# Performance work log

Hardware: AMD Instinct MI355X
Metric: run time of the kernel (lower is better)

## Reference

```python
import jax, jax.numpy as jnp
import numpy as np

NUM_HEADS = 16
EMBED_DIM = 128
SEQ_LEN = 1024
BATCH = 4


def setup_inputs() -> dict:
    key = jax.random.key(0)
    ks = jax.random.split(key, 5)
    x = jax.random.normal(ks[0], (BATCH, SEQ_LEN, EMBED_DIM), dtype=jnp.float32)
    scale = 0.02
    w_q = jax.random.normal(ks[1], (NUM_HEADS * EMBED_DIM, EMBED_DIM), dtype=jnp.float32) * scale
    w_k = jax.random.normal(ks[2], (NUM_HEADS * EMBED_DIM, EMBED_DIM), dtype=jnp.float32) * scale
    w_v = jax.random.normal(ks[3], (NUM_HEADS * EMBED_DIM, EMBED_DIM), dtype=jnp.float32) * scale
    w_o = jax.random.normal(ks[4], (EMBED_DIM, NUM_HEADS * EMBED_DIM), dtype=jnp.float32) * scale
    return {"x": x, "w_q": w_q, "w_k": w_k, "w_v": w_v, "w_o": w_o}


def _rope_tables(seq_len, embed_dim, dtype):
    half = embed_dim // 2
    # faithful to source: angles = 10000 ** (2*i / embed_dim)  (positive exponent)
    angles = jnp.power(jnp.asarray(10000.0, dtype), 2.0 * jnp.arange(half, dtype=dtype) / embed_dim)
    theta = jnp.arange(seq_len, dtype=dtype)[:, None] * angles[None, :]  # [S, half]
    return jnp.cos(theta), jnp.sin(theta)


def _apply_rope(t, cos, sin):
    # t: [B, S, H, E] viewed as complex pairs on last dim
    B, S, H, E = t.shape
    tr = t.reshape(B, S, H, E // 2, 2)
    a, b = tr[..., 0], tr[..., 1]
    c = cos[None, :, None, :]
    s = sin[None, :, None, :]
    out = jnp.stack([a * c - b * s, a * s + b * c], axis=-1)
    return out.reshape(B, S, H, E)


def reference(x, w_q, w_k, w_v, w_o):
    B, S, E = x.shape
    H = NUM_HEADS
    q = jnp.einsum('bse,fe->bsf', x, w_q).reshape(B, S, H, E)
    k = jnp.einsum('bse,fe->bsf', x, w_k).reshape(B, S, H, E)
    v = jnp.einsum('bse,fe->bsf', x, w_v).reshape(B, S, H, E)
    cos, sin = _rope_tables(S, E, x.dtype)
    q = _apply_rope(q, cos, sin)
    k = _apply_rope(k, cos, sin)
    att = jnp.einsum('bqhd,bkhd->bhqk', q, k) / jnp.sqrt(jnp.asarray(E, x.dtype))
    causal = jnp.tril(jnp.ones((S, S), dtype=bool))[None, None]
    att = jnp.where(causal, att, jnp.asarray(-jnp.inf, x.dtype))
    att = jax.nn.softmax(att, axis=-1)
    y = jnp.einsum('bhqk,bkhd->bqhd', att, v).reshape(B, S, H * E)
    return jnp.einsum('bsf,ef->bse', y, w_o)
```

## Files before the change

kernel.cpp:

```cpp
#include <hip/hip_runtime.h>

typedef unsigned short u16;
typedef unsigned int   u32;
typedef __attribute__((ext_vector_type(8))) short bf8_t;
typedef __attribute__((ext_vector_type(4))) float f4_t;

#define SEQ   1024
#define NH    16
#define DH    128
#define BATCH 4
#define MROWS 4096
#define FDIM  2048

__device__ __forceinline__ u16 f2bf(float f) {
  union { float f; u32 u; } v; v.f = f;
  u32 u = v.u;
  u += 0x7fffu + ((u >> 16) & 1u);
  return (u16)(u >> 16);
}

__global__ __launch_bounds__(256) void to_bf16(
    const float* __restrict__ x,  const float* __restrict__ wq,
    const float* __restrict__ wk, const float* __restrict__ wv,
    const float* __restrict__ wo,
    u16* __restrict__ xb, u16* __restrict__ wqb, u16* __restrict__ wkb,
    u16* __restrict__ wvb, u16* __restrict__ wob) {
  int i = blockIdx.x * 256 + threadIdx.x;
  const float* s; u16* d; int o;
  if      (i <  65536) { s = x;  d = xb;  o = i; }
  else if (i <  98304) { s = wq; d = wqb; o = i - 65536; }
  else if (i < 131072) { s = wk; d = wkb; o = i - 98304; }
  else if (i < 163840) { s = wv; d = wvb; o = i - 131072; }
  else                 { s = wo; d = wob; o = i - 163840; }
  const f4_t* sp = reinterpret_cast<const f4_t*>(s + (size_t)o * 8);
  f4_t a = sp[0], b = sp[1];
  bf8_t pk;
#pragma unroll
  for (int j = 0; j < 4; ++j) { pk[j] = (short)f2bf(a[j]); pk[4 + j] = (short)f2bf(b[j]); }
  *reinterpret_cast<bf8_t*>(d + (size_t)o * 8) = pk;
}

__global__ __launch_bounds__(256) void rope_tables(float* __restrict__ cosT,
                                                   float* __restrict__ sinT) {
  int i = blockIdx.x * 256 + threadIdx.x;
  int s = i >> 6, p = i & 63;
  float ef = (float)(2 * p) / 128.0f;
  float angf = (float)pow(10000.0, (double)ef);
  float thf  = (float)s * angf;
  cosT[i] = cosf(thf);
  sinT[i] = sinf(thf);
}

__global__ __launch_bounds__(256) void qkv_rope(
    const u16* __restrict__ xb,
    const u16* __restrict__ wqb, const u16* __restrict__ wkb,
    const u16* __restrict__ wvb,
    const float* __restrict__ cosT, const float* __restrict__ sinT,
    u16* __restrict__ qo, u16* __restrict__ ko, u16* __restrict__ vo) {
  __shared__ __align__(16) u16 a_lds[64 * 128];
  __shared__ __align__(16) u16 b_lds[64 * 128];
  const int tid = threadIdx.x;
  const int mt = blockIdx.x;
  const int by = blockIdx.y;
  const int mat = by >> 5;
  const int nt  = by & 31;
  const u16* w = (mat == 0) ? wqb : ((mat == 1) ? wkb : wvb);
  const int m0 = mt * 64, n0 = nt * 64;

#pragma unroll
  for (int i = 0; i < 4; ++i) {
    int idx = tid + i * 256;
    int row = idx >> 4, e0 = (idx & 15) * 8;
    int hw = ((row << 7) | e0) ^ ((row & 7) << 3);
    bf8_t xa = *reinterpret_cast<const bf8_t*>(xb + (size_t)(m0 + row) * 128 + e0);
    *reinterpret_cast<bf8_t*>(&a_lds[hw]) = xa;
    bf8_t wa = *reinterpret_cast<const bf8_t*>(w + (size_t)(n0 + row) * 128 + e0);
    *reinterpret_cast<bf8_t*>(&b_lds[hw]) = wa;
  }
  __syncthreads();

  const int lane = tid & 63, wid = tid >> 6;
  const int wr = wid >> 1, wc = wid & 1;
  const int g = lane >> 4, c16 = lane & 15;
  f4_t acc[2][2];
#pragma unroll
  for (int a = 0; a < 2; ++a)
#pragma unroll
    for (int b = 0; b < 2; ++b) acc[a][b] = (f4_t)0.0f;

#pragma unroll
  for (int kc = 0; kc < 4; ++kc) {
    bf8_t af[2], bf_[2];
#pragma unroll
    for (int fr = 0; fr < 2; ++fr) {
      int row = wr * 32 + fr * 16 + c16;
      int hw = ((row << 7) | (kc * 32 + g * 8)) ^ ((row & 7) << 3);
      af[fr] = *reinterpret_cast<const bf8_t*>(&a_lds[hw]);
    }
#pragma unroll
    for (int fc = 0; fc < 2; ++fc) {
      int row = wc * 32 + fc * 16 + c16;
      int hw = ((row << 7) | (kc * 32 + g * 8)) ^ ((row & 7) << 3);
      bf_[fc] = *reinterpret_cast<const bf8_t*>(&b_lds[hw]);
    }
#pragma unroll
    for (int fr = 0; fr < 2; ++fr)
#pragma unroll
      for (int fc = 0; fc < 2; ++fc)
        acc[fr][fc] = __builtin_amdgcn_mfma_f32_16x16x32_bf16(af[fr], bf_[fc], acc[fr][fc], 0, 0, 0);
  }

  if (mat == 2) {
    __syncthreads();
#pragma unroll
    for (int fr = 0; fr < 2; ++fr)
#pragma unroll
      for (int fc = 0; fc < 2; ++fc)
#pragma unroll
        for (int j = 0; j < 4; ++j) {
          int fcol = wc * 32 + fc * 16 + c16;
          int m = wr * 32 + fr * 16 + g * 4 + j;
          a_lds[fcol * 72 + m] = f2bf(acc[fr][fc][j]);
        }
    __syncthreads();
    const int b = mt >> 4, sl0 = m0 & 1023;
    const int hq = nt >> 1, dvb = (nt & 1) * 64;
#pragma unroll
    for (int i = 0; i < 2; ++i) {
      int r = tid >> 2, c0 = ((tid & 3) * 2 + i) * 8;
      bf8_t v = *reinterpret_cast<const bf8_t*>(&a_lds[r * 72 + c0]);
      size_t adr = ((size_t)((b * 16 + hq) * 128 + dvb + r)) * 1024 + sl0 + c0;
      *reinterpret_cast<bf8_t*>(vo + adr) = v;
    }
    return;
  }

  u16* outp = (mat == 0) ? qo : ko;
#pragma unroll
  for (int fr = 0; fr < 2; ++fr) {
#pragma unroll
    for (int fc = 0; fc < 2; ++fc) {
      int fcol = n0 + wc * 32 + fc * 16 + c16;
      int h = fcol >> 7, d = fcol & 127, p = d >> 1;
#pragma unroll
      for (int j = 0; j < 4; ++j) {
        int m = m0 + wr * 32 + fr * 16 + g * 4 + j;
        int b = m >> 10, sl = m & 1023;
        float v = acc[fr][fc][j];
        float vx = __shfl_xor(v, 1);
        float cv = cosT[sl * 64 + p], sv = sinT[sl * 64 + p];
        if (!(lane & 1)) {
          float e_out = v * cv - vx * sv;
          float o_out = v * sv + vx * cv;
          u32 u = (u32)f2bf(e_out) | ((u32)f2bf(o_out) << 16);
          u32 elem = ((u32)((b * 16 + h) * 1024 + sl)) * 128 + (u32)d;
          reinterpret_cast<u32*>(outp)[elem >> 1] = u;
        }
      }
    }
  }
}

__device__ __forceinline__ void stage_kv(const u16* __restrict__ Kp,
                                         const u16* __restrict__ Vt, int t,
                                         int tid, u16* k_lds, u16* vT) {
#pragma unroll
  for (int i = 0; i < 4; ++i) {
    int n = tid >> 2, c0 = ((tid & 3) * 4 + i) * 8;
    bf8_t kv = *reinterpret_cast<const bf8_t*>(Kp + (size_t)(t * 64 + n) * 128 + c0);
    *reinterpret_cast<bf8_t*>(&k_lds[n * 128 + (c0 ^ ((n & 7) << 3))]) = kv;
    int dv = tid >> 1, c1 = ((tid & 1) * 4 + i) * 8;
    bf8_t vv = *reinterpret_cast<const bf8_t*>(Vt + (size_t)dv * 1024 + t * 64 + c1);
    *reinterpret_cast<bf8_t*>(&vT[dv * 72 + c1]) = vv;
  }
}

__global__ __launch_bounds__(256, 3) void attn(
    const u16* __restrict__ qw, const u16* __restrict__ kw,
    const u16* __restrict__ vtg, u16* __restrict__ yw) {
  __shared__ __align__(16) u16 k_lds[64 * 128];
  __shared__ __align__(16) u16 vT[144 * 72];
  __shared__ __align__(16) u16 p_lds[4][16 * 64];
  const int tid = threadIdx.x, lane = tid & 63, wid = tid >> 6;
  const int g = lane >> 4, c16 = lane & 15;
  const int bid = blockIdx.x;
  const int pp = 15 - (bid >> 6);
  const int bh = bid & 63;
  const int b = bh >> 4, h = bh & 15;
  const int qt = 2 * pp + (wid >> 1);
  const int T = pp + 1;
  const u16* Qp = qw + (size_t)bh * SEQ * DH;
  const u16* Kp = kw + (size_t)bh * SEQ * DH;
  const u16* Vt = vtg + (size_t)bh * DH * SEQ;
  const float kscale = 0.08838834764831845f * 1.4426950408889634f;
  const int qrow0 = qt * 32 + (wid & 1) * 16;
  const int moff = (wid >> 1) * 32 + (wid & 1) * 16;

  {
    int r = 128 + (tid >> 4), c0 = (tid & 15) * 4;
    u16 v = (r == 128) ? (u16)0x3F80 : (u16)0;
#pragma unroll
    for (int e = 0; e < 4; ++e) vT[r * 72 + c0 + e] = v;
  }

  bf8_t qf[4];
#pragma unroll
  for (int c = 0; c < 4; ++c)
    qf[c] = *reinterpret_cast<const bf8_t*>(Qp + (size_t)(qrow0 + c16) * 128 + c * 32 + g * 8);

  f4_t yacc[9];
#pragma unroll
  for (int f = 0; f < 9; ++f) yacc[f] = (f4_t)0.0f;
  float m_run[4];
#pragma unroll
  for (int j = 0; j < 4; ++j) m_run[j] = -3e38f;

  stage_kv(Kp, Vt, 0, tid, k_lds, vT);
  __syncthreads();

  for (int t = 0; t < T; ++t) {
    f4_t sf[4];
#pragma unroll
    for (int nf = 0; nf < 4; ++nf) sf[nf] = (f4_t)0.0f;
    __builtin_amdgcn_s_setprio(1);
#pragma unroll
    for (int nf = 0; nf < 4; ++nf) {
      int row = nf * 16 + c16;
#pragma unroll
      for (int kc = 0; kc < 4; ++kc) {
        int hw = ((row << 7) | (kc * 32 + g * 8)) ^ ((row & 7) << 3);
        bf8_t kf = *reinterpret_cast<const bf8_t*>(&k_lds[hw]);
        sf[nf] = __builtin_amdgcn_mfma_f32_16x16x32_bf16(qf[kc], kf, sf[nf], 0, 0, 0);
      }
    }
    __builtin_amdgcn_s_setprio(0);

    if (t == T - 1) {
#pragma unroll
      for (int nf = 0; nf < 4; ++nf) {
        int keyc = nf * 16 + c16;
#pragma unroll
        for (int j = 0; j < 4; ++j)
          if (keyc > moff + g * 4 + j) sf[nf][j] = -3e38f;
      }
    }

    int chk = 0;
#pragma unroll
    for (int j = 0; j < 4; ++j) {
      float lmx = fmaxf(fmaxf(sf[0][j], sf[1][j]), fmaxf(sf[2][j], sf[3][j]));
      chk |= (lmx > m_run[j] + 32.0f) ? 1 : 0;
    }
    if (__any(chk)) {
      float lm[4];
#pragma unroll
      for (int j = 0; j < 4; ++j) {
        lm[j] = fmaxf(fmaxf(sf[0][j], sf[1][j]), fmaxf(sf[2][j], sf[3][j]));
        lm[j] = fmaxf(lm[j], __shfl_xor(lm[j], 1));
        lm[j] = fmaxf(lm[j], __shfl_xor(lm[j], 2));
        lm[j] = fmaxf(lm[j], __shfl_xor(lm[j], 4));
        lm[j] = fmaxf(lm[j], __shfl_xor(lm[j], 8));
      }
#pragma unroll
      for (int j = 0; j < 4; ++j) {
        float mn = fmaxf(m_run[j], lm[j]);
        float alpha = exp2f((m_run[j] - mn) * kscale);
        m_run[j] = mn;
#pragma unroll
        for (int f = 0; f < 9; ++f) yacc[f][j] *= alpha;
      }
    }

#pragma unroll
    for (int nf = 0; nf < 4; ++nf) {
#pragma unroll
      for (int j = 0; j < 4; ++j) {
        float pv = exp2f((sf[nf][j] - m_run[j]) * kscale);
        int q = g * 4 + j, n = nf * 16 + c16;
        int hw = ((q << 6) | n) ^ ((q & 7) << 3);
        p_lds[wid][hw] = f2bf(pv);
      }
    }
    bf8_t pa[2];
#pragma unroll
    for (int cc = 0; cc < 2; ++cc) {
      int hw = ((c16 << 6) | (cc * 32 + g * 8)) ^ ((c16 & 7) << 3);
      pa[cc] = *reinterpret_cast<const bf8_t*>(&p_lds[wid][hw]);
    }

    __builtin_amdgcn_s_setprio(1);
#pragma unroll
    for (int f = 0; f < 9; ++f) {
#pragma unroll
      for (int cc = 0; cc < 2; ++cc) {
        bf8_t vf = *reinterpret_cast<const bf8_t*>(&vT[(f * 16 + c16) * 72 + cc * 32 + g * 8]);
        yacc[f] = __builtin_amdgcn_mfma_f32_16x16x32_bf16(pa[cc], vf, yacc[f], 0, 0, 0);
      }
    }
    __builtin_amdgcn_s_setprio(0);

    __syncthreads();
    if (t + 1 < T) {
      stage_kv(Kp, Vt, t + 1, tid, k_lds, vT);
      __syncthreads();
    }
  }

  float rl[4];
#pragma unroll
  for (int j = 0; j < 4; ++j) {
    float lv = __shfl(yacc[8][j], lane & 48);
    rl[j] = 1.0f / lv;
  }
#pragma unroll
  for (int f = 0; f < 8; ++f) {
#pragma unroll
    for (int j = 0; j < 4; ++j) {
      float yv = yacc[f][j] * rl[j];
      float yn = __shfl_xor(yv, 1);
      if (!(lane & 1)) {
        int s_ = qrow0 + g * 4 + j;
        int dv = f * 16 + c16;
        u32 u = (u32)f2bf(yv) | ((u32)f2bf(yn) << 16);
        u32 elem = ((u32)(b * 1024 + s_)) * 2048 + (u32)(h * 128 + dv);
        reinterpret_cast<u32*>(yw)[elem >> 1] = u;
      }
    }
  }
}

__global__ __launch_bounds__(256) void oproj(
    const u16* __restrict__ yw, const u16* __restrict__ wob,
    float* __restrict__ out) {
  __shared__ __align__(16) u16 a_lds[64 * 64];
  __shared__ __align__(16) u16 b_lds[64 * 64];
  const int tid = threadIdx.x, lane = tid & 63, wid = tid >> 6;
  const int g = lane >> 4, c16 = lane & 15;
  const int wr = wid >> 1, wc = wid & 1;
  const int m0 = blockIdx.x * 64, n0 = blockIdx.y * 64;
  const int z = blockIdx.z;
  f4_t acc[2][2];
#pragma unroll
  for (int a = 0; a < 2; ++a)
#pragma unroll
    for (int b = 0; b < 2; ++b) acc[a][b] = (f4_t)0.0f;

  for (int kt = z * 16; kt < z * 16 + 16; ++kt) {
    int kb = kt * 64;
#pragma unroll
    for (int i = 0; i < 2; ++i) {
      int idx = tid + i * 256;
      int row = idx >> 3, k0 = (idx & 7) * 8;
      int hw = ((row << 6) | k0) ^ ((row & 7) << 3);
      bf8_t av = *reinterpret_cast<const bf8_t*>(yw + (size_t)(m0 + row) * 2048 + kb + k0);
      *reinterpret_cast<bf8_t*>(&a_lds[hw]) = av;
      bf8_t bv = *reinterpret_cast<const bf8_t*>(wob + (size_t)(n0 + row) * 2048 + kb + k0);
      *reinterpret_cast<bf8_t*>(&b_lds[hw]) = bv;
    }
    __syncthreads();
#pragma unroll
    for (int c = 0; c < 2; ++c) {
      bf8_t af[2], bf_[2];
#pragma unroll
      for (int fr = 0; fr < 2; ++fr) {
        int row = wr * 32 + fr * 16 + c16;
        int hw = ((row << 6) | (c * 32 + g * 8)) ^ ((row & 7) << 3);
        af[fr] = *reinterpret_cast<const bf8_t*>(&a_lds[hw]);
      }
#pragma unroll
      for (int fc = 0; fc < 2; ++fc) {
        int row = wc * 32 + fc * 16 + c16;
        int hw = ((row << 6) | (c * 32 + g * 8)) ^ ((row & 7) << 3);
        bf_[fc] = *reinterpret_cast<const bf8_t*>(&b_lds[hw]);
      }
#pragma unroll
      for (int fr = 0; fr < 2; ++fr)
#pragma unroll
        for (int fc = 0; fc < 2; ++fc)
          acc[fr][fc] = __builtin_amdgcn_mfma_f32_16x16x32_bf16(af[fr], bf_[fc], acc[fr][fc], 0, 0, 0);
    }
    __syncthreads();
  }
#pragma unroll
  for (int fr = 0; fr < 2; ++fr)
#pragma unroll
    for (int fc = 0; fc < 2; ++fc)
#pragma unroll
      for (int j = 0; j < 4; ++j) {
        int m = m0 + wr * 32 + fr * 16 + g * 4 + j;
        int e = n0 + wc * 32 + fc * 16 + c16;
        atomicAdd(&out[(size_t)m * 128 + e], acc[fr][fc][j]);
      }
}

extern "C" void kernel_launch(void* const* d_in, const int* in_sizes, int n_in,
                              void* d_out, int out_size, void* d_ws, size_t ws_size,
                              hipStream_t stream) {
  const float* x  = (const float*)d_in[0];
  const float* wq = (const float*)d_in[1];
  const float* wk = (const float*)d_in[2];
  const float* wv = (const float*)d_in[3];
  const float* wo = (const float*)d_in[4];
  float* out = (float*)d_out;

  char* ws = (char*)d_ws;
  const size_t NEED = (512ull << 10) + 4ull * (16ull << 20) + (3ull << 20);
  if (ws_size < NEED) return;
  float* cosT = (float*)ws;
  float* sinT = cosT + 64 * 1024;
  u16* qws = (u16*)(ws + (512 << 10));
  u16* kws = qws + (8u << 20);
  u16* vws = kws + (8u << 20);
  u16* yws = vws + (8u << 20);
  u16* xb  = yws + (8u << 20);
  u16* wqb = xb  + (1u << 19);
  u16* wkb = wqb + (1u << 18);
  u16* wvb = wkb + (1u << 18);
  u16* wob = wvb + (1u << 18);

  hipMemsetAsync(d_out, 0, (size_t)out_size * sizeof(float), stream);
  to_bf16<<<768, 256, 0, stream>>>(x, wq, wk, wv, wo, xb, wqb, wkb, wvb, wob);
  rope_tables<<<256, 256, 0, stream>>>(cosT, sinT);
  qkv_rope<<<dim3(64, 96), 256, 0, stream>>>(xb, wqb, wkb, wvb, cosT, sinT, qws, kws, vws);
  attn<<<1024, 256, 0, stream>>>(qws, kws, vws, yws);
  oproj<<<dim3(64, 2, 2), 256, 0, stream>>>(yws, wob, out);
}
```

Measured before the change: 99.16 us.

## Fuse prep kernels, transpose rope tables, register-prefetch K/V and oproj tiles

Merges the bf16 conversion and rope-table kernels into one launch, which saves one kernel launch. The rope tables become position-major per frequency so the qkv epilogue can fetch four consecutive cos/sin values with one vector load. In attention and oproj, the next tile's global loads are issued into registers before the current tile's MFMA work and written to LDS afterwards, so load latency overlaps compute. The cost is extra registers, which may reduce occupancy in the attention kernel, which is bounded at 3 blocks.

After: 100.6 us. About the same (+1.4%).

```diff
diff --git a/kernel.cpp b/kernel.cpp
--- a/kernel.cpp
+++ b/kernel.cpp
@@ -19,36 +19,37 @@
   return (u16)(u >> 16);
 }
 
-__global__ __launch_bounds__(256) void to_bf16(
+__global__ __launch_bounds__(256) void prep(
     const float* __restrict__ x,  const float* __restrict__ wq,
     const float* __restrict__ wk, const float* __restrict__ wv,
     const float* __restrict__ wo,
     u16* __restrict__ xb, u16* __restrict__ wqb, u16* __restrict__ wkb,
-    u16* __restrict__ wvb, u16* __restrict__ wob) {
-  int i = blockIdx.x * 256 + threadIdx.x;
-  const float* s; u16* d; int o;
-  if      (i <  65536) { s = x;  d = xb;  o = i; }
-  else if (i <  98304) { s = wq; d = wqb; o = i - 65536; }
-  else if (i < 131072) { s = wk; d = wkb; o = i - 98304; }
-  else if (i < 163840) { s = wv; d = wvb; o = i - 131072; }
-  else                 { s = wo; d = wob; o = i - 163840; }
-  const f4_t* sp = reinterpret_cast<const f4_t*>(s + (size_t)o * 8);
-  f4_t a = sp[0], b = sp[1];
-  bf8_t pk;
-#pragma unroll
-  for (int j = 0; j < 4; ++j) { pk[j] = (short)f2bf(a[j]); pk[4 + j] = (short)f2bf(b[j]); }
-  *reinterpret_cast<bf8_t*>(d + (size_t)o * 8) = pk;
-}
-
-__global__ __launch_bounds__(256) void rope_tables(float* __restrict__ cosT,
-                                                   float* __restrict__ sinT) {
-  int i = blockIdx.x * 256 + threadIdx.x;
-  int s = i >> 6, p = i & 63;
-  float ef = (float)(2 * p) / 128.0f;
-  float angf = (float)pow(10000.0, (double)ef);
-  float thf  = (float)s * angf;
-  cosT[i] = cosf(thf);
-  sinT[i] = sinf(thf);
+    u16* __restrict__ wvb, u16* __restrict__ wob,
+    float* __restrict__ cosT, float* __restrict__ sinT) {
+  const int gb = blockIdx.x;
+  if (gb < 768) {
+    int i = gb * 256 + threadIdx.x;
+    const float* s; u16* d; int o;
+    if      (i <  65536) { s = x;  d = xb;  o = i; }
+    else if (i <  98304) { s = wq; d = wqb; o = i - 65536; }
+    else if (i < 131072) { s = wk; d = wkb; o = i - 98304; }
+    else if (i < 163840) { s = wv; d = wvb; o = i - 131072; }
+    else                 { s = wo; d = wob; o = i - 163840; }
+    const f4_t* sp = reinterpret_cast<const f4_t*>(s + (size_t)o * 8);
+    f4_t a = sp[0], b = sp[1];
+    bf8_t pk;
+#pragma unroll
+    for (int j = 0; j < 4; ++j) { pk[j] = (short)f2bf(a[j]); pk[4 + j] = (short)f2bf(b[j]); }
+    *reinterpret_cast<bf8_t*>(d + (size_t)o * 8) = pk;
+  } else {
+    int i = (gb - 768) * 256 + threadIdx.x;
+    int p = i >> 10, s = i & 1023;
+    float ef = (float)(2 * p) / 128.0f;
+    float angf = (float)pow(10000.0, (double)ef);
+    float thf  = (float)s * angf;
+    cosT[i] = cosf(thf);
+    sinT[i] = sinf(thf);
+  }
 }
 
 __global__ __launch_bounds__(256) void qkv_rope(
@@ -142,18 +143,20 @@
     for (int fc = 0; fc < 2; ++fc) {
       int fcol = n0 + wc * 32 + fc * 16 + c16;
       int h = fcol >> 7, d = fcol & 127, p = d >> 1;
+      int m_base = m0 + wr * 32 + fr * 16 + g * 4;
+      int b = m_base >> 10, sl_base = m_base & 1023;
+      f4_t cv4 = *reinterpret_cast<const f4_t*>(&cosT[p * 1024 + sl_base]);
+      f4_t sv4 = *reinterpret_cast<const f4_t*>(&sinT[p * 1024 + sl_base]);
 #pragma unroll
       for (int j = 0; j < 4; ++j) {
-        int m = m0 + wr * 32 + fr * 16 + g * 4 + j;
-        int b = m >> 10, sl = m & 1023;
         float v = acc[fr][fc][j];
         float vx = __shfl_xor(v, 1);
-        float cv = cosT[sl * 64 + p], sv = sinT[sl * 64 + p];
+        float cv = cv4[j], sv = sv4[j];
         if (!(lane & 1)) {
           float e_out = v * cv - vx * sv;
           float o_out = v * sv + vx * cv;
           u32 u = (u32)f2bf(e_out) | ((u32)f2bf(o_out) << 16);
-          u32 elem = ((u32)((b * 16 + h) * 1024 + sl)) * 128 + (u32)d;
+          u32 elem = ((u32)((b * 16 + h) * 1024 + (sl_base + j))) * 128 + (u32)d;
           reinterpret_cast<u32*>(outp)[elem >> 1] = u;
         }
       }
@@ -161,17 +164,26 @@
   }
 }
 
-__device__ __forceinline__ void stage_kv(const u16* __restrict__ Kp,
-                                         const u16* __restrict__ Vt, int t,
-                                         int tid, u16* k_lds, u16* vT) {
+__device__ __forceinline__ void stage_load(const u16* __restrict__ Kp,
+                                           const u16* __restrict__ Vt, int t,
+                                           int tid, bf8_t kreg[4], bf8_t vreg[4]) {
 #pragma unroll
   for (int i = 0; i < 4; ++i) {
     int n = tid >> 2, c0 = ((tid & 3) * 4 + i) * 8;
-    bf8_t kv = *reinterpret_cast<const bf8_t*>(Kp + (size_t)(t * 64 + n) * 128 + c0);
-    *reinterpret_cast<bf8_t*>(&k_lds[n * 128 + (c0 ^ ((n & 7) << 3))]) = kv;
+    kreg[i] = *reinterpret_cast<const bf8_t*>(Kp + (size_t)(t * 64 + n) * 128 + c0);
     int dv = tid >> 1, c1 = ((tid & 1) * 4 + i) * 8;
-    bf8_t vv = *reinterpret_cast<const bf8_t*>(Vt + (size_t)dv * 1024 + t * 64 + c1);
-    *reinterpret_cast<bf8_t*>(&vT[dv * 72 + c1]) = vv;
+    vreg[i] = *reinterpret_cast<const bf8_t*>(Vt + (size_t)dv * 1024 + t * 64 + c1);
+  }
+}
+__device__ __forceinline__ void stage_write(int tid, const bf8_t kreg[4],
+                                            const bf8_t vreg[4],
+                                            u16* k_lds, u16* vT) {
+#pragma unroll
+  for (int i = 0; i < 4; ++i) {
+    int n = tid >> 2, c0 = ((tid & 3) * 4 + i) * 8;
+    *reinterpret_cast<bf8_t*>(&k_lds[n * 128 + (c0 ^ ((n & 7) << 3))]) = kreg[i];
+    int dv = tid >> 1, c1 = ((tid & 1) * 4 + i) * 8;
+    *reinterpret_cast<bf8_t*>(&vT[dv * 72 + c1]) = vreg[i];
   }
 }
 
@@ -215,10 +227,18 @@
 #pragma unroll
   for (int j = 0; j < 4; ++j) m_run[j] = -3e38f;
 
-  stage_kv(Kp, Vt, 0, tid, k_lds, vT);
+  {
+    bf8_t k0[4], v0[4];
+    stage_load(Kp, Vt, 0, tid, k0, v0);
+    stage_write(tid, k0, v0, k_lds, vT);
+  }
   __syncthreads();
 
   for (int t = 0; t < T; ++t) {
+    const bool pf = (t + 1 < T);
+    bf8_t kreg[4], vreg[4];
+    if (pf) stage_load(Kp, Vt, t + 1, tid, kreg, vreg);
+
     f4_t sf[4];
 #pragma unroll
     for (int nf = 0; nf < 4; ++nf) sf[nf] = (f4_t)0.0f;
@@ -300,8 +320,8 @@
     __builtin_amdgcn_s_setprio(0);
 
     __syncthreads();
-    if (t + 1 < T) {
-      stage_kv(Kp, Vt, t + 1, tid, k_lds, vT);
+    if (pf) {
+      stage_write(tid, kreg, vreg, k_lds, vT);
       __syncthreads();
     }
   }
@@ -339,25 +359,42 @@
   const int wr = wid >> 1, wc = wid & 1;
   const int m0 = blockIdx.x * 64, n0 = blockIdx.y * 64;
   const int z = blockIdx.z;
+  const int kt0 = z * 16;
   f4_t acc[2][2];
 #pragma unroll
   for (int a = 0; a < 2; ++a)
 #pragma unroll
     for (int b = 0; b < 2; ++b) acc[a][b] = (f4_t)0.0f;
 
-  for (int kt = z * 16; kt < z * 16 + 16; ++kt) {
-    int kb = kt * 64;
-#pragma unroll
-    for (int i = 0; i < 2; ++i) {
-      int idx = tid + i * 256;
-      int row = idx >> 3, k0 = (idx & 7) * 8;
-      int hw = ((row << 6) | k0) ^ ((row & 7) << 3);
-      bf8_t av = *reinterpret_cast<const bf8_t*>(yw + (size_t)(m0 + row) * 2048 + kb + k0);
-      *reinterpret_cast<bf8_t*>(&a_lds[hw]) = av;
-      bf8_t bv = *reinterpret_cast<const bf8_t*>(wob + (size_t)(n0 + row) * 2048 + kb + k0);
-      *reinterpret_cast<bf8_t*>(&b_lds[hw]) = bv;
-    }
-    __syncthreads();
+  const int srow = tid >> 3, sk0 = (tid & 7) * 8;
+
+  bf8_t areg[2], breg[2];
+#pragma unroll
+  for (int i = 0; i < 2; ++i) {
+    int row = srow + i * 32;
+    areg[i] = *reinterpret_cast<const bf8_t*>(yw + (size_t)(m0 + row) * 2048 + kt0 * 64 + sk0);
+    breg[i] = *reinterpret_cast<const bf8_t*>(wob + (size_t)(n0 + row) * 2048 + kt0 * 64 + sk0);
+  }
+#pragma unroll
+  for (int i = 0; i < 2; ++i) {
+    int row = srow + i * 32;
+    int hw = ((row << 6) | sk0) ^ ((row & 7) << 3);
+    *reinterpret_cast<bf8_t*>(&a_lds[hw]) = areg[i];
+    *reinterpret_cast<bf8_t*>(&b_lds[hw]) = breg[i];
+  }
+  __syncthreads();
+
+  for (int kt = kt0; kt < kt0 + 16; ++kt) {
+    const bool pf = (kt + 1 < kt0 + 16);
+    if (pf) {
+      int kb = (kt + 1) * 64;
+#pragma unroll
+      for (int i = 0; i < 2; ++i) {
+        int row = srow + i * 32;
+        areg[i] = *reinterpret_cast<const bf8_t*>(yw + (size_t)(m0 + row) * 2048 + kb + sk0);
+        breg[i] = *reinterpret_cast<const bf8_t*>(wob + (size_t)(n0 + row) * 2048 + kb + sk0);
+      }
+    }
 #pragma unroll
     for (int c = 0; c < 2; ++c) {
       bf8_t af[2], bf_[2];
@@ -380,6 +417,16 @@
           acc[fr][fc] = __builtin_amdgcn_mfma_f32_16x16x32_bf16(af[fr], bf_[fc], acc[fr][fc], 0, 0, 0);
     }
     __syncthreads();
+    if (pf) {
+#pragma unroll
+      for (int i = 0; i < 2; ++i) {
+        int row = srow + i * 32;
+        int hw = ((row << 6) | sk0) ^ ((row & 7) << 3);
+        *reinterpret_cast<bf8_t*>(&a_lds[hw]) = areg[i];
+        *reinterpret_cast<bf8_t*>(&b_lds[hw]) = breg[i];
+      }
+      __syncthreads();
+    }
   }
 #pragma unroll
   for (int fr = 0; fr < 2; ++fr)
@@ -419,8 +466,7 @@
   u16* wob = wvb + (1u << 18);
 
   hipMemsetAsync(d_out, 0, (size_t)out_size * sizeof(float), stream);
-  to_bf16<<<768, 256, 0, stream>>>(x, wq, wk, wv, wo, xb, wqb, wkb, wvb, wob);
-  rope_tables<<<256, 256, 0, stream>>>(cosT, sinT);
+  prep<<<1024, 256, 0, stream>>>(x, wq, wk, wv, wo, xb, wqb, wkb, wvb, wob, cosT, sinT);
   qkv_rope<<<dim3(64, 96), 256, 0, stream>>>(xb, wqb, wkb, wvb, cosT, sinT, qws, kws, vws);
   attn<<<1024, 256, 0, stream>>>(qws, kws, vws, yws);
   oproj<<<dim3(64, 2, 2), 256, 0, stream>>>(yws, wob, out);
```
